# Kernel optimization log

Hardware: AMD Instinct MI355X
Metric: run time of the kernel (lower is better)

Reference implementation:

```python
import jax, jax.numpy as jnp
import numpy as np

TAU = 0.07
EPS = 1e-12  # matches torch F.normalize default eps


def setup_inputs() -> dict:
    key = jax.random.key(0)
    k1, k2 = jax.random.split(key)
    B, C, H, W, K = 4, 256, 256, 256, 19
    feat = jax.random.normal(k1, (B, C, H, W), dtype=jnp.float32)
    # binary ground-truth one-hot-ish masks; gt.eq(1) selects positives
    gt = jax.random.randint(k2, (B, K, H, W), 0, 2).astype(jnp.float32)
    return {"feat": feat, "gt": gt}


def _l2norm(x, axis):
    n = jnp.sqrt(jnp.sum(x * x, axis=axis, keepdims=True))
    return x / jnp.maximum(n, EPS)


def reference(feat, gt):
    # feat: [B,C,H,W], gt: [B,K,H,W] binary
    pos = (gt == 1.0).astype(feat.dtype)              # [B,K,H,W]
    fnorm = _l2norm(feat, axis=1)                     # per-pixel L2 normalize over C
    # scatter-add normalized features into class prototypes
    k0 = jnp.einsum('bkhw,bchw->kc', pos, fnorm)      # [K,C]
    k0n = _l2norm(k0, axis=1)                         # [K,C]
    # prototype-vs-pixel similarities, softmax over classes
    logits = jnp.einsum('kc,bchw->bkhw', k0n, fnorm) / TAU  # [B,K,H,W]
    logp = jax.nn.log_softmax(logits, axis=1)
    num_pos = jnp.sum(pos)
    loss = -jnp.sum(pos * logp) / num_pos
    return loss
```

## Files before the change

kernel.cpp:

```cpp
#include <hip/hip_runtime.h>
#include <math.h>

namespace {
constexpr int Cn = 256;
constexpr int Kn = 19;
constexpr int HW = 256 * 256;
constexpr int P  = 4 * HW;
constexpr float TAUv = 0.07f;
constexpr float EPSv = 1e-12f;

constexpr int K0_OFF   = 0;
constexpr int K0N_OFF  = 4864;
constexpr int SUMS_OFF = 9728;
constexpr int ZERO_N   = 9730;
constexpr int P1_GRID  = 1024;
constexpr int P3_GRID  = P / 256;
}

__global__ __launch_bounds__(256) void gc_init(float* __restrict__ ws) {
  int i = blockIdx.x * 256 + threadIdx.x;
  if (i < ZERO_N) ws[i] = 0.0f;
}

__global__ __launch_bounds__(256, 4) void gc_phase1(const float* __restrict__ feat,
                                                    const float* __restrict__ gt,
                                                    float* __restrict__ k0) {
  __shared__ float tile[32 * 256];
  __shared__ float part[256];
  __shared__ float wls[32][20];

  const int t = threadIdx.x;
  const int p = t & 31;
  const int g = t >> 5;

  float acc[Kn];
#pragma unroll
  for (int k = 0; k < Kn; k++) acc[k] = 0.0f;

  for (int tid = blockIdx.x; tid < P / 32; tid += gridDim.x) {
    const int p0  = tid << 5;
    const int b   = p0 >> 16;
    const int hw0 = p0 & (HW - 1);
    const float* fb = feat + (size_t)b * (Cn * HW) + hw0;

    __syncthreads();

    float v[32];
#pragma unroll
    for (int j = 0; j < 32; j++) v[j] = fb[(size_t)((g << 5) + j) * HW + p];
    float ss = 0.0f;
#pragma unroll
    for (int j = 0; j < 32; j++) {
      const int c = (g << 5) + j;
      ss += v[j] * v[j];
      tile[(p << 8) + (c ^ p)] = v[j];
    }
    part[t] = ss;

    unsigned msk = 0;
    if (t < 32) {
      const float* gb = gt + (size_t)b * (Kn * HW) + hw0 + p;
#pragma unroll
      for (int k = 0; k < Kn; k++)
        msk |= (gb[(size_t)k * HW] == 1.0f) ? (1u << k) : 0u;
    }

    __syncthreads();

    if (t < 32) {
      float fss = 0.0f;
#pragma unroll
      for (int q = 0; q < 8; q++) fss += part[(q << 5) + p];
      const float rn = 1.0f / fmaxf(sqrtf(fss), EPSv);
#pragma unroll
      for (int k = 0; k < Kn; k++) wls[p][k] = ((msk >> k) & 1u) ? rn : 0.0f;
      wls[p][19] = 0.0f;
    }

    __syncthreads();

#pragma unroll 4
    for (int pp = 0; pp < 32; pp++) {
      const float4 w0 = *(const float4*)&wls[pp][0];
      const float4 w1 = *(const float4*)&wls[pp][4];
      const float4 w2 = *(const float4*)&wls[pp][8];
      const float4 w3 = *(const float4*)&wls[pp][12];
      const float4 w4 = *(const float4*)&wls[pp][16];
      const float fv = tile[(pp << 8) + (t ^ pp)];
      acc[0]  = fmaf(fv, w0.x, acc[0]);  acc[1]  = fmaf(fv, w0.y, acc[1]);
      acc[2]  = fmaf(fv, w0.z, acc[2]);  acc[3]  = fmaf(fv, w0.w, acc[3]);
      acc[4]  = fmaf(fv, w1.x, acc[4]);  acc[5]  = fmaf(fv, w1.y, acc[5]);
      acc[6]  = fmaf(fv, w1.z, acc[6]);  acc[7]  = fmaf(fv, w1.w, acc[7]);
      acc[8]  = fmaf(fv, w2.x, acc[8]);  acc[9]  = fmaf(fv, w2.y, acc[9]);
      acc[10] = fmaf(fv, w2.z, acc[10]); acc[11] = fmaf(fv, w2.w, acc[11]);
      acc[12] = fmaf(fv, w3.x, acc[12]); acc[13] = fmaf(fv, w3.y, acc[13]);
      acc[14] = fmaf(fv, w3.z, acc[14]); acc[15] = fmaf(fv, w3.w, acc[15]);
      acc[16] = fmaf(fv, w4.x, acc[16]); acc[17] = fmaf(fv, w4.y, acc[17]);
      acc[18] = fmaf(fv, w4.z, acc[18]);
    }
  }

#pragma unroll
  for (int k = 0; k < Kn; k++) atomicAdd(&k0[k * 256 + t], acc[k]);
}

__global__ __launch_bounds__(256) void gc_phase2(const float* __restrict__ k0,
                                                 float* __restrict__ k0n) {
  const int lane = threadIdx.x & 63;
  const int wv   = threadIdx.x >> 6;
  for (int r = wv; r < Kn; r += 4) {
    float s = 0.0f;
#pragma unroll
    for (int j = 0; j < 4; j++) {
      const float v = k0[r * 256 + (j << 6) + lane];
      s += v * v;
    }
#pragma unroll
    for (int off = 32; off > 0; off >>= 1) s += __shfl_down(s, off);
    s = __shfl(s, 0);
    const float rn = 1.0f / fmaxf(sqrtf(s), EPSv);
#pragma unroll
    for (int j = 0; j < 4; j++) {
      const int c = (j << 6) + lane;
      k0n[r * 256 + c] = k0[r * 256 + c] * rn;
    }
  }
}

__global__ __launch_bounds__(256, 4) void gc_phase3(const float* __restrict__ feat,
                                                    const float* __restrict__ gt,
                                                    const float* __restrict__ k0n,
                                                    float* __restrict__ sums) {
  __shared__ float wco[Kn * 256];
  __shared__ float tile[16 * 256];

  const int t = threadIdx.x;
#pragma unroll
  for (int i = 0; i < Kn; i++) wco[i * 256 + t] = k0n[i * 256 + t];

  const int pix0 = blockIdx.x << 8;
  const int b    = pix0 >> 16;
  const int hw   = (pix0 & (HW - 1)) + t;
  const float* fb = feat + (size_t)b * (Cn * HW) + hw;

  float dot[Kn];
#pragma unroll
  for (int k = 0; k < Kn; k++) dot[k] = 0.0f;
  float ss = 0.0f;

  float v[16];
#pragma unroll
  for (int j = 0; j < 16; j++) v[j] = fb[(size_t)j * HW];

  for (int c0 = 0; c0 < Cn; c0 += 16) {
    __syncthreads();
#pragma unroll
    for (int j = 0; j < 16; j++) tile[j * 256 + t] = v[j];
    __syncthreads();

    if (c0 + 16 < Cn) {
#pragma unroll
      for (int j = 0; j < 16; j++) v[j] = fb[(size_t)(c0 + 16 + j) * HW];
    }

#pragma unroll
    for (int j4 = 0; j4 < 16; j4 += 4) {
      const float f0 = tile[(j4 + 0) * 256 + t];
      const float f1 = tile[(j4 + 1) * 256 + t];
      const float f2 = tile[(j4 + 2) * 256 + t];
      const float f3 = tile[(j4 + 3) * 256 + t];
      ss = fmaf(f0, f0, ss); ss = fmaf(f1, f1, ss);
      ss = fmaf(f2, f2, ss); ss = fmaf(f3, f3, ss);
#pragma unroll
      for (int k = 0; k < Kn; k++) {
        const float4 w = *(const float4*)&wco[k * 256 + c0 + j4];
        dot[k] = fmaf(f3, w.w, fmaf(f2, w.z, fmaf(f1, w.y, fmaf(f0, w.x, dot[k]))));
      }
    }
  }

  const float sc = 1.0f / (fmaxf(sqrtf(ss), EPSv) * TAUv);
  float mx = -1e30f;
#pragma unroll
  for (int k = 0; k < Kn; k++) { dot[k] *= sc; mx = fmaxf(mx, dot[k]); }
  float se = 0.0f;
#pragma unroll
  for (int k = 0; k < Kn; k++) se += __expf(dot[k] - mx);
  const float lse = __logf(se) + mx;

  const float* gb = gt + (size_t)b * (Kn * HW) + hw;
  float lsum = 0.0f, npos = 0.0f;
#pragma unroll
  for (int k = 0; k < Kn; k++) {
    if (gb[(size_t)k * HW] == 1.0f) { lsum += lse - dot[k]; npos += 1.0f; }
  }

#pragma unroll
  for (int off = 32; off > 0; off >>= 1) {
    lsum += __shfl_down(lsum, off);
    npos += __shfl_down(npos, off);
  }
  if ((t & 63) == 0) {
    atomicAdd(&sums[0], lsum);
    atomicAdd(&sums[1], npos);
  }
}

__global__ void gc_finalize(const float* __restrict__ sums, float* __restrict__ out) {
  if (threadIdx.x == 0 && blockIdx.x == 0)
    out[0] = sums[0] / sums[1];
}

extern "C" void kernel_launch(void* const* d_in, const int* in_sizes, int n_in,
                              void* d_out, int out_size, void* d_ws, size_t ws_size,
                              hipStream_t stream) {
  const float* feat = (const float*)d_in[0];
  const float* gt   = (const float*)d_in[1];
  float* ws  = (float*)d_ws;
  float* out = (float*)d_out;

  float* k0   = ws + K0_OFF;
  float* k0n  = ws + K0N_OFF;
  float* sums = ws + SUMS_OFF;

  gc_init<<<dim3((ZERO_N + 255) / 256), dim3(256), 0, stream>>>(ws);
  gc_phase1<<<dim3(P1_GRID), dim3(256), 0, stream>>>(feat, gt, k0);
  gc_phase2<<<dim3(1), dim3(256), 0, stream>>>(k0, k0n);
  gc_phase3<<<dim3(P3_GRID), dim3(256), 0, stream>>>(feat, gt, k0n, sums);
  gc_finalize<<<dim3(1), dim3(64), 0, stream>>>(sums, out);
}
```

Measured before the change: 602.0 us.

## Register-block both GEMM phases and drop shared tile staging in phase 3

Phase 1 now splits the 32 pixels of each tile across four waves. Each thread owns four channels via float4 shared reads, so it keeps 76 accumulators and writes to four per-wave partial prototype buffers, which phase 2 sums. Phase 3 drops the shared-memory feature tile and its barriers, and each thread processes two pixels directly from registers with software prefetch, halving the grid. The aim is fewer LDS round trips and syncs and more reuse of each weight load, at the cost of much higher register pressure, which may lower occupancy or cause spills.

```diff
diff --git a/kernel.cpp b/kernel.cpp
--- a/kernel.cpp
+++ b/kernel.cpp
@@ -9,12 +9,13 @@
 constexpr float TAUv = 0.07f;
 constexpr float EPSv = 1e-12f;
 
-constexpr int K0_OFF   = 0;
-constexpr int K0N_OFF  = 4864;
-constexpr int SUMS_OFF = 9728;
-constexpr int ZERO_N   = 9730;
+constexpr int K0X4_OFF = 0;
+constexpr int K0N_OFF  = 4 * Kn * 256;
+constexpr int SUMS_OFF = K0N_OFF + Kn * 256;
+constexpr int ZERO_N   = SUMS_OFF + 2;
 constexpr int P1_GRID  = 1024;
-constexpr int P3_GRID  = P / 256;
+constexpr int P3_GRID  = P / 512;
+constexpr int TROW     = 260;
 }
 
 __global__ __launch_bounds__(256) void gc_init(float* __restrict__ ws) {
@@ -22,38 +23,43 @@
   if (i < ZERO_N) ws[i] = 0.0f;
 }
 
-__global__ __launch_bounds__(256, 4) void gc_phase1(const float* __restrict__ feat,
-                                                    const float* __restrict__ gt,
-                                                    float* __restrict__ k0) {
-  __shared__ float tile[32 * 256];
+__global__ __launch_bounds__(256) void gc_phase1(const float* __restrict__ feat,
+                                                 const float* __restrict__ gt,
+                                                 float* __restrict__ k0x4) {
+  __shared__ float tile[32 * TROW];
   __shared__ float part[256];
   __shared__ float wls[32][20];
 
   const int t = threadIdx.x;
   const int p = t & 31;
   const int g = t >> 5;
-
-  float acc[Kn];
-#pragma unroll
-  for (int k = 0; k < Kn; k++) acc[k] = 0.0f;
+  const int L = t & 63;
+  const int w = t >> 6;
+
+  float acc[Kn * 4];
+#pragma unroll
+  for (int i = 0; i < Kn * 4; i++) acc[i] = 0.0f;
 
   for (int tid = blockIdx.x; tid < P / 32; tid += gridDim.x) {
     const int p0  = tid << 5;
     const int b   = p0 >> 16;
     const int hw0 = p0 & (HW - 1);
-    const float* fb = feat + (size_t)b * (Cn * HW) + hw0;
+    const float* fb = feat + (size_t)b * (Cn * HW) + hw0 + p;
 
     __syncthreads();
 
-    float v[32];
-#pragma unroll
-    for (int j = 0; j < 32; j++) v[j] = fb[(size_t)((g << 5) + j) * HW + p];
     float ss = 0.0f;
 #pragma unroll
-    for (int j = 0; j < 32; j++) {
-      const int c = (g << 5) + j;
-      ss += v[j] * v[j];
-      tile[(p << 8) + (c ^ p)] = v[j];
+    for (int h = 0; h < 2; h++) {
+      float v[16];
+#pragma unroll
+      for (int j = 0; j < 16; j++) v[j] = fb[(size_t)((g << 5) + (h << 4) + j) * HW];
+#pragma unroll
+      for (int j = 0; j < 16; j++) ss = fmaf(v[j], v[j], ss);
+#pragma unroll
+      for (int q = 0; q < 4; q++)
+        *(float4*)&tile[p * TROW + (g << 5) + (h << 4) + (q << 2)] =
+            make_float4(v[q * 4], v[q * 4 + 1], v[q * 4 + 2], v[q * 4 + 3]);
     }
     part[t] = ss;
 
@@ -79,41 +85,57 @@
 
     __syncthreads();
 
-#pragma unroll 4
-    for (int pp = 0; pp < 32; pp++) {
+#pragma unroll
+    for (int i = 0; i < 8; i++) {
+      const int pp = (w << 3) + i;
+      const float4 f  = *(const float4*)&tile[pp * TROW + (L << 2)];
       const float4 w0 = *(const float4*)&wls[pp][0];
       const float4 w1 = *(const float4*)&wls[pp][4];
       const float4 w2 = *(const float4*)&wls[pp][8];
       const float4 w3 = *(const float4*)&wls[pp][12];
       const float4 w4 = *(const float4*)&wls[pp][16];
-      const float fv = tile[(pp << 8) + (t ^ pp)];
-      acc[0]  = fmaf(fv, w0.x, acc[0]);  acc[1]  = fmaf(fv, w0.y, acc[1]);
-      acc[2]  = fmaf(fv, w0.z, acc[2]);  acc[3]  = fmaf(fv, w0.w, acc[3]);
-      acc[4]  = fmaf(fv, w1.x, acc[4]);  acc[5]  = fmaf(fv, w1.y, acc[5]);
-      acc[6]  = fmaf(fv, w1.z, acc[6]);  acc[7]  = fmaf(fv, w1.w, acc[7]);
-      acc[8]  = fmaf(fv, w2.x, acc[8]);  acc[9]  = fmaf(fv, w2.y, acc[9]);
-      acc[10] = fmaf(fv, w2.z, acc[10]); acc[11] = fmaf(fv, w2.w, acc[11]);
-      acc[12] = fmaf(fv, w3.x, acc[12]); acc[13] = fmaf(fv, w3.y, acc[13]);
-      acc[14] = fmaf(fv, w3.z, acc[14]); acc[15] = fmaf(fv, w3.w, acc[15]);
-      acc[16] = fmaf(fv, w4.x, acc[16]); acc[17] = fmaf(fv, w4.y, acc[17]);
-      acc[18] = fmaf(fv, w4.z, acc[18]);
-    }
-  }
-
-#pragma unroll
-  for (int k = 0; k < Kn; k++) atomicAdd(&k0[k * 256 + t], acc[k]);
-}
-
-__global__ __launch_bounds__(256) void gc_phase2(const float* __restrict__ k0,
+      const float wk[19] = {w0.x,w0.y,w0.z,w0.w, w1.x,w1.y,w1.z,w1.w,
+                            w2.x,w2.y,w2.z,w2.w, w3.x,w3.y,w3.z,w3.w,
+                            w4.x,w4.y,w4.z};
+#pragma unroll
+      for (int k = 0; k < Kn; k++) {
+        acc[k * 4 + 0] = fmaf(f.x, wk[k], acc[k * 4 + 0]);
+        acc[k * 4 + 1] = fmaf(f.y, wk[k], acc[k * 4 + 1]);
+        acc[k * 4 + 2] = fmaf(f.z, wk[k], acc[k * 4 + 2]);
+        acc[k * 4 + 3] = fmaf(f.w, wk[k], acc[k * 4 + 3]);
+      }
+    }
+  }
+
+  float* k0w = k0x4 + (size_t)w * (Kn * 256);
+#pragma unroll
+  for (int k = 0; k < Kn; k++) {
+#pragma unroll
+    for (int j = 0; j < 4; j++)
+      atomicAdd(&k0w[k * 256 + (L << 2) + j], acc[k * 4 + j]);
+  }
+}
+
+__global__ __launch_bounds__(256) void gc_phase2(const float* __restrict__ k0x4,
                                                  float* __restrict__ k0n) {
-  const int lane = threadIdx.x & 63;
-  const int wv   = threadIdx.x >> 6;
+  __shared__ float ks[Kn * 256];
+  const int t = threadIdx.x;
+#pragma unroll
+  for (int k = 0; k < Kn; k++) {
+    float s = 0.0f;
+#pragma unroll
+    for (int w = 0; w < 4; w++) s += k0x4[w * (Kn * 256) + k * 256 + t];
+    ks[k * 256 + t] = s;
+  }
+  __syncthreads();
+  const int lane = t & 63;
+  const int wv   = t >> 6;
   for (int r = wv; r < Kn; r += 4) {
     float s = 0.0f;
 #pragma unroll
     for (int j = 0; j < 4; j++) {
-      const float v = k0[r * 256 + (j << 6) + lane];
-      s += v * v;
+      const float v = ks[r * 256 + (j << 6) + lane];
+      s = fmaf(v, v, s);
     }
 #pragma unroll
     for (int off = 32; off > 0; off >>= 1) s += __shfl_down(s, off);
@@ -122,77 +144,95 @@
 #pragma unroll
     for (int j = 0; j < 4; j++) {
       const int c = (j << 6) + lane;
-      k0n[r * 256 + c] = k0[r * 256 + c] * rn;
-    }
-  }
-}
-
-__global__ __launch_bounds__(256, 4) void gc_phase3(const float* __restrict__ feat,
-                                                    const float* __restrict__ gt,
-                                                    const float* __restrict__ k0n,
-                                                    float* __restrict__ sums) {
+      k0n[r * 256 + c] = ks[r * 256 + c] * rn;
+    }
+  }
+}
+
+__global__ __launch_bounds__(256) void gc_phase3(const float* __restrict__ feat,
+                                                 const float* __restrict__ gt,
+                                                 const float* __restrict__ k0n,
+                                                 float* __restrict__ sums) {
   __shared__ float wco[Kn * 256];
-  __shared__ float tile[16 * 256];
 
   const int t = threadIdx.x;
 #pragma unroll
   for (int i = 0; i < Kn; i++) wco[i * 256 + t] = k0n[i * 256 + t];
 
-  const int pix0 = blockIdx.x << 8;
+  const int pix0 = blockIdx.x << 9;
   const int b    = pix0 >> 16;
   const int hw   = (pix0 & (HW - 1)) + t;
   const float* fb = feat + (size_t)b * (Cn * HW) + hw;
 
-  float dot[Kn];
-#pragma unroll
-  for (int k = 0; k < Kn; k++) dot[k] = 0.0f;
-  float ss = 0.0f;
-
-  float v[16];
-#pragma unroll
-  for (int j = 0; j < 16; j++) v[j] = fb[(size_t)j * HW];
-
-  for (int c0 = 0; c0 < Cn; c0 += 16) {
-    __syncthreads();
-#pragma unroll
-    for (int j = 0; j < 16; j++) tile[j * 256 + t] = v[j];
-    __syncthreads();
-
-    if (c0 + 16 < Cn) {
-#pragma unroll
-      for (int j = 0; j < 16; j++) v[j] = fb[(size_t)(c0 + 16 + j) * HW];
-    }
-
-#pragma unroll
-    for (int j4 = 0; j4 < 16; j4 += 4) {
-      const float f0 = tile[(j4 + 0) * 256 + t];
-      const float f1 = tile[(j4 + 1) * 256 + t];
-      const float f2 = tile[(j4 + 2) * 256 + t];
-      const float f3 = tile[(j4 + 3) * 256 + t];
-      ss = fmaf(f0, f0, ss); ss = fmaf(f1, f1, ss);
-      ss = fmaf(f2, f2, ss); ss = fmaf(f3, f3, ss);
-#pragma unroll
-      for (int k = 0; k < Kn; k++) {
-        const float4 w = *(const float4*)&wco[k * 256 + c0 + j4];
-        dot[k] = fmaf(f3, w.w, fmaf(f2, w.z, fmaf(f1, w.y, fmaf(f0, w.x, dot[k]))));
+  float dot0[Kn], dot1[Kn];
+#pragma unroll
+  for (int k = 0; k < Kn; k++) { dot0[k] = 0.0f; dot1[k] = 0.0f; }
+  float ss0 = 0.0f, ss1 = 0.0f;
+
+  float ca[8], cb[8];
+#pragma unroll
+  for (int j = 0; j < 8; j++) {
+    ca[j] = fb[(size_t)j * HW];
+    cb[j] = fb[(size_t)j * HW + 256];
+  }
+  __syncthreads();
+
+  for (int c0 = 0; c0 < Cn; c0 += 8) {
+    float na[8], nb[8];
+    if (c0 + 8 < Cn) {
+#pragma unroll
+      for (int j = 0; j < 8; j++) {
+        na[j] = fb[(size_t)(c0 + 8 + j) * HW];
+        nb[j] = fb[(size_t)(c0 + 8 + j) * HW + 256];
       }
     }
-  }
-
-  const float sc = 1.0f / (fmaxf(sqrtf(ss), EPSv) * TAUv);
-  float mx = -1e30f;
-#pragma unroll
-  for (int k = 0; k < Kn; k++) { dot[k] *= sc; mx = fmaxf(mx, dot[k]); }
-  float se = 0.0f;
-#pragma unroll
-  for (int k = 0; k < Kn; k++) se += __expf(dot[k] - mx);
-  const float lse = __logf(se) + mx;
+#pragma unroll
+    for (int j = 0; j < 8; j++) {
+      ss0 = fmaf(ca[j], ca[j], ss0);
+      ss1 = fmaf(cb[j], cb[j], ss1);
+    }
+#pragma unroll
+    for (int k = 0; k < Kn; k++) {
+      const float4 w0 = *(const float4*)&wco[k * 256 + c0];
+      const float4 w1 = *(const float4*)&wco[k * 256 + c0 + 4];
+      float d0 = dot0[k], d1 = dot1[k];
+      d0 = fmaf(ca[0], w0.x, d0); d0 = fmaf(ca[1], w0.y, d0);
+      d0 = fmaf(ca[2], w0.z, d0); d0 = fmaf(ca[3], w0.w, d0);
+      d0 = fmaf(ca[4], w1.x, d0); d0 = fmaf(ca[5], w1.y, d0);
+      d0 = fmaf(ca[6], w1.z, d0); d0 = fmaf(ca[7], w1.w, d0);
+      d1 = fmaf(cb[0], w0.x, d1); d1 = fmaf(cb[1], w0.y, d1);
+      d1 = fmaf(cb[2], w0.z, d1); d1 = fmaf(cb[3], w0.w, d1);
+      d1 = fmaf(cb[4], w1.x, d1); d1 = fmaf(cb[5], w1.y, d1);
+      d1 = fmaf(cb[6], w1.z, d1); d1 = fmaf(cb[7], w1.w, d1);
+      dot0[k] = d0; dot1[k] = d1;
+    }
+#pragma unroll
+    for (int j = 0; j < 8; j++) { ca[j] = na[j]; cb[j] = nb[j]; }
+  }
+
+  const float sc0 = 1.0f / (fmaxf(sqrtf(ss0), EPSv) * TAUv);
+  const float sc1 = 1.0f / (fmaxf(sqrtf(ss1), EPSv) * TAUv);
+  float mx0 = -1e30f, mx1 = -1e30f;
+#pragma unroll
+  for (int k = 0; k < Kn; k++) {
+    dot0[k] *= sc0; mx0 = fmaxf(mx0, dot0[k]);
+    dot1[k] *= sc1; mx1 = fmaxf(mx1, dot1[k]);
+  }
+  float se0 = 0.0f, se1 = 0.0f;
+#pragma unroll
+  for (int k = 0; k < Kn; k++) {
+    se0 += __expf(dot0[k] - mx0);
+    se1 += __expf(dot1[k] - mx1);
+  }
+  const float lse0 = __logf(se0) + mx0;
+  const float lse1 = __logf(se1) + mx1;
 
   const float* gb = gt + (size_t)b * (Kn * HW) + hw;
   float lsum = 0.0f, npos = 0.0f;
 #pragma unroll
   for (int k = 0; k < Kn; k++) {
-    if (gb[(size_t)k * HW] == 1.0f) { lsum += lse - dot[k]; npos += 1.0f; }
+    if (gb[(size_t)k * HW] == 1.0f)       { lsum += lse0 - dot0[k]; npos += 1.0f; }
+    if (gb[(size_t)k * HW + 256] == 1.0f) { lsum += lse1 - dot1[k]; npos += 1.0f; }
   }
 
 #pragma unroll
@@ -219,13 +259,13 @@
   float* ws  = (float*)d_ws;
   float* out = (float*)d_out;
 
-  float* k0   = ws + K0_OFF;
+  float* k0x4 = ws + K0X4_OFF;
   float* k0n  = ws + K0N_OFF;
   float* sums = ws + SUMS_OFF;
 
   gc_init<<<dim3((ZERO_N + 255) / 256), dim3(256), 0, stream>>>(ws);
-  gc_phase1<<<dim3(P1_GRID), dim3(256), 0, stream>>>(feat, gt, k0);
-  gc_phase2<<<dim3(1), dim3(256), 0, stream>>>(k0, k0n);
+  gc_phase1<<<dim3(P1_GRID), dim3(256), 0, stream>>>(feat, gt, k0x4);
+  gc_phase2<<<dim3(1), dim3(256), 0, stream>>>(k0x4, k0n);
   gc_phase3<<<dim3(P3_GRID), dim3(256), 0, stream>>>(feat, gt, k0n, sums);
   gc_finalize<<<dim3(1), dim3(64), 0, stream>>>(sums, out);
 }
```

Result: slower. 841.7 us (+39.8%).
